# Kernel tuning notes

Hardware: AMD Instinct MI355X
Metric: run time of the kernel (lower is better)

## Reference

```python
import jax, jax.numpy as jnp
import numpy as np

NUM_HEADS = 4


def setup_inputs() -> dict:
    key = jax.random.key(0)
    ks = jax.random.split(key, 5)
    B, N, D = 4096, 49, 128  # B = batch(64) * num_windows(64), N = 7*7 window
    nW = 64
    x = jax.random.normal(ks[0], (B, N, D), dtype=jnp.float32)
    mask = jax.random.normal(ks[1], (nW, N, N), dtype=jnp.float32)
    w_qkv = jax.random.normal(ks[2], (3 * D, D), dtype=jnp.float32) * 0.02
    w_proj = jax.random.normal(ks[3], (D, D), dtype=jnp.float32) * 0.02
    b_proj = jax.random.normal(ks[4], (D,), dtype=jnp.float32) * 0.02
    return {"x": x, "mask": mask, "w_qkv": w_qkv, "w_proj": w_proj, "b_proj": b_proj}


def reference(x, mask, w_qkv, w_proj, b_proj):
    B, N, D = x.shape
    H = NUM_HEADS
    hd = D // H
    scale = hd ** (-0.5)
    # qkv projection (torch Linear: y = x @ W^T), no bias
    qkv = (x @ w_qkv.T).reshape(B, N, 3, H, hd)
    qkv = jnp.transpose(qkv, (2, 0, 3, 1, 4))  # [3, B, H, N, hd]
    q, k, v = qkv[0], qkv[1], qkv[2]
    attn = jnp.einsum("bhqd,bhkd->bhqk", q, k) * scale  # [B, H, N, N]
    nW = mask.shape[0]
    # add per-window additive mask, broadcast over batch and heads
    attn = attn.reshape(B // nW, nW, H, N, N) + mask[None, :, None, :, :]
    attn = attn.reshape(B, H, N, N)
    attn = jax.nn.softmax(attn, axis=-1)
    out = jnp.einsum("bhqk,bhkd->bhqd", attn, v)  # [B, H, N, hd]
    out = jnp.transpose(out, (0, 2, 1, 3)).reshape(B, N, D)
    return out @ w_proj.T + b_proj
```

## Files before the change

### kernel.cpp

```cpp
#include <hip/hip_runtime.h>
#include <hip/hip_bf16.h>

typedef _Float16 f16;
typedef __attribute__((ext_vector_type(8))) _Float16 f16x8;
typedef __attribute__((ext_vector_type(4))) _Float16 f16x4;
typedef __attribute__((ext_vector_type(4))) float f32x4;

#define MFMA16(a, b, c) __builtin_amdgcn_mfma_f32_16x16x32_f16((a), (b), (c), 0, 0, 0)

#define NWIN 4096
#define WPB 16

__global__ void cvt_weights(const float* __restrict__ wq,
                            const float* __restrict__ wp,
                            f16* __restrict__ o) {
    int i = blockIdx.x * blockDim.x + threadIdx.x;
    if (i < 49152) o[i] = (f16)wq[i];
    if (i < 16384) o[49152 + i] = (f16)wp[i];
}

__device__ inline f16x8 cvt8(const float* p) {
    float4 u0 = *(const float4*)p;
    float4 u1 = *(const float4*)(p + 4);
    f16x8 t;
    t[0] = (f16)u0.x; t[1] = (f16)u0.y; t[2] = (f16)u0.z; t[3] = (f16)u0.w;
    t[4] = (f16)u1.x; t[5] = (f16)u1.y; t[6] = (f16)u1.z; t[7] = (f16)u1.w;
    return t;
}

__global__ __launch_bounds__(512, 1)
void fused_all(const float* __restrict__ x, const float* __restrict__ mask,
               const f16* __restrict__ wq_h, const f16* __restrict__ wp_h,
               const float* __restrict__ bias, float* __restrict__ out) {
    __shared__ f16 xb[2][64 * 128];
    __shared__ f16 qlds[64 * 128];
    __shared__ f16 klds[64 * 128];
    __shared__ f16 vlds[128 * 64];
    __shared__ f16 scr[8][2048];

    const int tid = threadIdx.x;
    const int wave = tid >> 6;
    const int lane = tid & 63;
    const int lg = lane >> 4;
    const int lr = lane & 15;
    const int w0 = blockIdx.x * WPB;

    const int amt = wave & 3;
    const int ahh = wave >> 2;
    const int ar0 = amt * 16;

    f16* ps0 = scr[wave];
    f16* ps1 = scr[wave] + 1024;

    f16x8 bw[3][4];
#pragma unroll
    for (int j = 0; j < 3; ++j)
#pragma unroll
        for (int kc = 0; kc < 4; ++kc)
            bw[j][kc] = *(const f16x8*)&wq_h[((wave + 8 * j) * 16 + lr) * 128 + kc * 32 + 8 * lg];
    f16x8 wpr[4];
#pragma unroll
    for (int kc = 0; kc < 4; ++kc)
        wpr[kc] = *(const f16x8*)&wp_h[(wave * 16 + lr) * 128 + kc * 32 + 8 * lg];
    const float bc = bias[wave * 16 + lr];

    auto stage = [&](int w, int p) {
        const float* xw = x + (size_t)w * (49 * 128);
        for (int i = tid; i < 2048; i += 512) {
            const int row = i >> 5;
            const int c4 = (i & 31) << 2;
            float4 v = {0.f, 0.f, 0.f, 0.f};
            if (row < 49) v = ((const float4*)xw)[i];
            f16x4 t;
            t[0] = (f16)v.x; t[1] = (f16)v.y; t[2] = (f16)v.z; t[3] = (f16)v.w;
            *(f16x4*)&xb[p][row * 128 + (c4 ^ ((row & 7) << 3))] = t;
        }
    };

    stage(w0, 0);
    __syncthreads();

    const float sc = 0.17677669529663687f;

    for (int wi = 0; wi < WPB; ++wi) {
        const int w = w0 + wi;
        const int cur = wi & 1;
        if (wi < WPB - 1) stage(w + 1, cur ^ 1);

        const float* mw = mask + (size_t)(w & 63) * (49 * 49);
        float mv[4][4];
#pragma unroll
        for (int reg = 0; reg < 4; ++reg) {
            const int n = ar0 + 4 * lg + reg;
#pragma unroll
            for (int nt = 0; nt < 4; ++nt) {
                const int col = nt * 16 + lr;
                mv[reg][nt] = (n < 49 && col < 49) ? mw[n * 49 + col] : 0.f;
            }
        }

#pragma unroll
        for (int mt = 0; mt < 4; ++mt) {
            const int nb = mt * 16;
            f16x8 a[4];
#pragma unroll
            for (int kc = 0; kc < 4; ++kc)
                a[kc] = *(const f16x8*)&xb[cur][(nb + lr) * 128 + ((kc * 32 + 8 * lg) ^ ((lr & 7) << 3))];

#pragma unroll
            for (int j = 0; j < 3; ++j) {
                __builtin_amdgcn_s_setprio(1);
                f32x4 acc = {0.f, 0.f, 0.f, 0.f};
#pragma unroll
                for (int kc = 0; kc < 4; ++kc) acc = MFMA16(a[kc], bw[j][kc], acc);
                __builtin_amdgcn_s_setprio(0);

                const int c = wave * 16 + lr;
                if (j < 2) {
                    f16* dst = (j == 0) ? qlds : klds;
#pragma unroll
                    for (int reg = 0; reg < 4; ++reg) {
                        const int n = nb + 4 * lg + reg;
                        dst[n * 128 + (c ^ ((n & 7) << 3))] = (f16)acc[reg];
                    }
                } else {
#pragma unroll
                    for (int reg = 0; reg < 4; ++reg) {
                        const int n = nb + 4 * lg + reg;
                        vlds[c * 64 + (n ^ ((c & 7) << 3))] = (f16)acc[reg];
                    }
                }
            }
        }
        __syncthreads();

        const int h0 = 2 * ahh;
        const int h1 = 2 * ahh + 1;
        const int arow = ar0 + lr;

        f16x8 aq0 = *(const f16x8*)&qlds[arow * 128 + ((h0 * 32 + 8 * lg) ^ ((arow & 7) << 3))];
        f16x8 aq1 = *(const f16x8*)&qlds[arow * 128 + ((h1 * 32 + 8 * lg) ^ ((arow & 7) << 3))];

        f32x4 s0[4], s1[4];
        {
            __builtin_amdgcn_s_setprio(1);
#pragma unroll
            for (int nt = 0; nt < 4; ++nt) {
                const int krow = nt * 16 + lr;
                f16x8 bk = *(const f16x8*)&klds[krow * 128 + ((h0 * 32 + 8 * lg) ^ ((krow & 7) << 3))];
                f32x4 z = {0.f, 0.f, 0.f, 0.f};
                s0[nt] = MFMA16(aq0, bk, z);
            }
#pragma unroll
            for (int nt = 0; nt < 4; ++nt) {
                const int krow = nt * 16 + lr;
                f16x8 bk = *(const f16x8*)&klds[krow * 128 + ((h1 * 32 + 8 * lg) ^ ((krow & 7) << 3))];
                f32x4 z = {0.f, 0.f, 0.f, 0.f};
                s1[nt] = MFMA16(aq1, bk, z);
            }
            __builtin_amdgcn_s_setprio(0);
        }

        float lsum0[4], lsum1[4];
#pragma unroll
        for (int reg = 0; reg < 4; ++reg) {
            const int row = 4 * lg + reg;
            float sum0 = 0.f, sum1 = 0.f;
#pragma unroll
            for (int nt = 0; nt < 4; ++nt) {
                const int col = nt * 16 + lr;
                const int off = row * 64 + (col ^ ((row & 7) << 3));
                float e0 = (col < 49) ? __expf(s0[nt][reg] * sc + mv[reg][nt]) : 0.f;
                float e1 = (col < 49) ? __expf(s1[nt][reg] * sc + mv[reg][nt]) : 0.f;
                sum0 += e0;
                sum1 += e1;
                ps0[off] = (f16)e0;
                ps1[off] = (f16)e1;
            }
            lsum0[reg] = sum0;
            lsum1[reg] = sum1;
        }

        f16x8 bv0[2][2], bv1[2][2];
#pragma unroll
        for (int nt = 0; nt < 2; ++nt)
#pragma unroll
            for (int kc = 0; kc < 2; ++kc) {
                const int vr0 = h0 * 32 + nt * 16 + lr;
                const int vr1 = h1 * 32 + nt * 16 + lr;
                bv0[nt][kc] = *(const f16x8*)&vlds[vr0 * 64 + ((kc * 32 + 8 * lg) ^ ((vr0 & 7) << 3))];
                bv1[nt][kc] = *(const f16x8*)&vlds[vr1 * 64 + ((kc * 32 + 8 * lg) ^ ((vr1 & 7) << 3))];
            }

        f16x8 ap0[2], ap1[2];
#pragma unroll
        for (int kc = 0; kc < 2; ++kc) {
            const int off = lr * 64 + ((kc * 32 + 8 * lg) ^ ((lr & 7) << 3));
            ap0[kc] = *(const f16x8*)&ps0[off];
            ap1[kc] = *(const f16x8*)&ps1[off];
        }
        f32x4 o00 = {0.f, 0.f, 0.f, 0.f}, o01 = {0.f, 0.f, 0.f, 0.f};
        f32x4 o10 = {0.f, 0.f, 0.f, 0.f}, o11 = {0.f, 0.f, 0.f, 0.f};
        __builtin_amdgcn_s_setprio(1);
#pragma unroll
        for (int kc = 0; kc < 2; ++kc) {
            o00 = MFMA16(ap0[kc], bv0[0][kc], o00);
            o01 = MFMA16(ap0[kc], bv0[1][kc], o01);
            o10 = MFMA16(ap1[kc], bv1[0][kc], o10);
            o11 = MFMA16(ap1[kc], bv1[1][kc], o11);
        }
        __builtin_amdgcn_s_setprio(0);

#pragma unroll
        for (int reg = 0; reg < 4; ++reg) {
            float sum0 = lsum0[reg], sum1 = lsum1[reg];
            for (int d = 1; d < 16; d <<= 1) {
                sum0 += __shfl_xor(sum0, d, 64);
                sum1 += __shfl_xor(sum1, d, 64);
            }
            const float inv0 = __fdividef(1.f, sum0);
            const float inv1 = __fdividef(1.f, sum1);
            o00[reg] *= inv0;
            o01[reg] *= inv0;
            o10[reg] *= inv1;
            o11[reg] *= inv1;
        }

#pragma unroll
        for (int reg = 0; reg < 4; ++reg) {
            const int n = ar0 + 4 * lg + reg;
            const int s = (n & 7) << 3;
            qlds[n * 128 + ((h0 * 32 + lr) ^ s)] = (f16)o00[reg];
            qlds[n * 128 + ((h0 * 32 + 16 + lr) ^ s)] = (f16)o01[reg];
            qlds[n * 128 + ((h1 * 32 + lr) ^ s)] = (f16)o10[reg];
            qlds[n * 128 + ((h1 * 32 + 16 + lr) ^ s)] = (f16)o11[reg];
        }
        __syncthreads();

        float* ob = out + (size_t)w * (49 * 128);
#pragma unroll
        for (int mt = 0; mt < 4; ++mt) {
            const int prow = mt * 16 + lr;
            f16x8 aa[4];
#pragma unroll
            for (int kc = 0; kc < 4; ++kc)
                aa[kc] = *(const f16x8*)&qlds[prow * 128 + ((kc * 32 + 8 * lg) ^ ((prow & 7) << 3))];
            __builtin_amdgcn_s_setprio(1);
            f32x4 acc = {0.f, 0.f, 0.f, 0.f};
#pragma unroll
            for (int kc = 0; kc < 4; ++kc) acc = MFMA16(aa[kc], wpr[kc], acc);
            __builtin_amdgcn_s_setprio(0);

#pragma unroll
            for (int reg = 0; reg < 4; ++reg) {
                const int n = mt * 16 + 4 * lg + reg;
                if (n < 49) ob[n * 128 + wave * 16 + lr] = acc[reg] + bc;
            }
        }
        __syncthreads();
    }
}

template <bool WB>
__global__ __launch_bounds__(256, 4)
void fused_wattn(const float* __restrict__ x, const float* __restrict__ mask,
                 const float* __restrict__ wq_f, const float* __restrict__ wp_f,
                 const f16* __restrict__ wq_h, const f16* __restrict__ wp_h,
                 const float* __restrict__ bias, float* __restrict__ out) {
    __shared__ f16 ks[64 * 128];
    __shared__ f16 vt[128 * 64];
    __shared__ f16 scr[4][1024];

    const int b = blockIdx.x;
    const int wid = b & 63;
    const int tid = threadIdx.x;
    const int wave = tid >> 6;
    const int lane = tid & 63;
    const int lg = lane >> 4;
    const int lr = lane & 15;
    const int r0 = wave * 16;
    f16* ps = scr[wave];

    f16x8 a[4];
    {
        const int xrow = r0 + lr;
        if (xrow < 49) {
            const float* xp = x + ((size_t)b * 49 + xrow) * 128 + 8 * lg;
#pragma unroll
            for (int kc = 0; kc < 4; ++kc) a[kc] = cvt8(xp + kc * 32);
        } else {
            f16x8 z = {0, 0, 0, 0, 0, 0, 0, 0};
#pragma unroll
            for (int kc = 0; kc < 4; ++kc) a[kc] = z;
        }
    }

    float mv[4][4];
#pragma unroll
    for (int reg = 0; reg < 4; ++reg) {
        const int n = r0 + 4 * lg + reg;
#pragma unroll
        for (int nt = 0; nt < 4; ++nt) {
            const int col = nt * 16 + lr;
            mv[reg][nt] = (n < 49 && col < 49) ? mask[((size_t)wid * 49 + n) * 49 + col] : 0.f;
        }
    }

    f16x4 qd[8];
#pragma unroll
    for (int ct = 0; ct < 24; ++ct) {
        const int wrow = ct * 16 + lr;
        f16x8 bw[4];
        if (WB) {
#pragma unroll
            for (int kc = 0; kc < 4; ++kc)
                bw[kc] = *(const f16x8*)&wq_h[wrow * 128 + kc * 32 + 8 * lg];
        } else {
#pragma unroll
            for (int kc = 0; kc < 4; ++kc)
                bw[kc] = cvt8(&wq_f[wrow * 128 + kc * 32 + 8 * lg]);
        }
        f32x4 acc = {0.f, 0.f, 0.f, 0.f};
#pragma unroll
        for (int kc = 0; kc < 4; ++kc) acc = MFMA16(a[kc], bw[kc], acc);

        if (ct < 8) {
            f16x4 q;
#pragma unroll
            for (int reg = 0; reg < 4; ++reg) q[reg] = (f16)acc[reg];
            qd[ct] = q;
        } else if (ct < 16) {
#pragma unroll
            for (int reg = 0; reg < 4; ++reg) {
                const int n = r0 + 4 * lg + reg;
                const int c = wrow - 128;
                ks[n * 128 + (c ^ ((n & 7) << 3))] = (f16)acc[reg];
            }
        } else {
#pragma unroll
            for (int reg = 0; reg < 4; ++reg) {
                const int n = r0 + 4 * lg + reg;
                const int dch = wrow - 256;
                vt[dch * 64 + (n ^ ((dch & 7) << 3))] = (f16)acc[reg];
            }
        }
    }
    __syncthreads();

    const float sc = 0.17677669529663687f;
    f32x4 oacc[4][2];

#pragma unroll
    for (int h = 0; h < 4; ++h) {
#pragma unroll
        for (int c2 = 0; c2 < 2; ++c2)
#pragma unroll
            for (int reg = 0; reg < 4; ++reg) {
                const int row = 4 * lg + reg;
                const int col = c2 * 16 + lr;
                ps[row * 32 + (col ^ ((row & 3) << 3))] = qd[2 * h + c2][reg];
            }
        f16x8 aq = *(const f16x8*)&ps[lr * 32 + ((8 * lg) ^ ((lr & 3) << 3))];

        f32x4 s[4];
#pragma unroll
        for (int nt = 0; nt < 4; ++nt) {
            const int krow = nt * 16 + lr;
            f16x8 bk = *(const f16x8*)&ks[krow * 128 + ((h * 32 + 8 * lg) ^ ((krow & 7) << 3))];
            f32x4 z = {0.f, 0.f, 0.f, 0.f};
            s[nt] = MFMA16(aq, bk, z);
        }

#pragma unroll
        for (int reg = 0; reg < 4; ++reg) {
            float vals[4];
            float sum = 0.f;
#pragma unroll
            for (int nt = 0; nt < 4; ++nt) {
                const int col = nt * 16 + lr;
                float e = (col < 49) ? __expf(s[nt][reg] * sc + mv[reg][nt]) : 0.f;
                vals[nt] = e;
                sum += e;
            }
            for (int d = 1; d < 16; d <<= 1) sum += __shfl_xor(sum, d, 64);
            const float inv = __fdividef(1.f, sum);
            const int row = 4 * lg + reg;
#pragma unroll
            for (int nt = 0; nt < 4; ++nt) {
                const int col = nt * 16 + lr;
                ps[row * 64 + (col ^ ((row & 7) << 3))] = (f16)(vals[nt] * inv);
            }
        }

        f16x8 ap[2];
#pragma unroll
        for (int kc = 0; kc < 2; ++kc)
            ap[kc] = *(const f16x8*)&ps[lr * 64 + ((kc * 32 + 8 * lg) ^ ((lr & 7) << 3))];
#pragma unroll
        for (int nt = 0; nt < 2; ++nt) {
            const int vrow = h * 32 + nt * 16 + lr;
            f32x4 acc = {0.f, 0.f, 0.f, 0.f};
#pragma unroll
            for (int kc = 0; kc < 2; ++kc) {
                f16x8 bv = *(const f16x8*)&vt[vrow * 64 + ((kc * 32 + 8 * lg) ^ ((vrow & 7) << 3))];
                acc = MFMA16(ap[kc], bv, acc);
            }
            oacc[h][nt] = acc;
        }
    }

    f16x8 aa[4];
#pragma unroll
    for (int pass = 0; pass < 2; ++pass) {
#pragma unroll
        for (int h2 = 0; h2 < 2; ++h2)
#pragma unroll
            for (int nt = 0; nt < 2; ++nt)
#pragma unroll
                for (int reg = 0; reg < 4; ++reg) {
                    const int row = 4 * lg + reg;
                    const int col = h2 * 32 + nt * 16 + lr;
                    ps[row * 64 + (col ^ ((row & 7) << 3))] = (f16)oacc[pass * 2 + h2][nt][reg];
                }
#pragma unroll
        for (int kcg = 0; kcg < 2; ++kcg)
            aa[pass * 2 + kcg] = *(const f16x8*)&ps[lr * 64 + ((kcg * 32 + 8 * lg) ^ ((lr & 7) << 3))];
    }

    float* ob = out + (size_t)b * (49 * 128);
#pragma unroll
    for (int ct = 0; ct < 8; ++ct) {
        const int wrow = ct * 16 + lr;
        f16x8 bw[4];
        if (WB) {
#pragma unroll
            for (int kc = 0; kc < 4; ++kc)
                bw[kc] = *(const f16x8*)&wq_h[wrow * 128 + kc * 32 + 8 * lg];
        } else {
#pragma unroll
            for (int kc = 0; kc < 4; ++kc)
                bw[kc] = cvt8(&wp_f[wrow * 128 + kc * 32 + 8 * lg]);
        }
        f32x4 acc = {0.f, 0.f, 0.f, 0.f};
#pragma unroll
        for (int kc = 0; kc < 4; ++kc) acc = MFMA16(aa[kc], bw[kc], acc);

        const float bc = bias[wrow];
#pragma unroll
        for (int reg = 0; reg < 4; ++reg) {
            const int n = r0 + 4 * lg + reg;
            if (n < 49) ob[n * 128 + ct * 16 + lr] = acc[reg] + bc;
        }
    }
}

extern "C" void kernel_launch(void* const* d_in, const int* in_sizes, int n_in,
                              void* d_out, int out_size, void* d_ws, size_t ws_size,
                              hipStream_t stream) {
    const float* x = (const float*)d_in[0];
    const float* mask = (const float*)d_in[1];
    const float* wq = (const float*)d_in[2];
    const float* wp = (const float*)d_in[3];
    const float* bp = (const float*)d_in[4];
    float* out = (float*)d_out;

    const size_t need_wb = (size_t)(49152 + 16384) * sizeof(f16);

    if (ws_size >= need_wb && d_ws != nullptr) {
        f16* wsh = (f16*)d_ws;
        cvt_weights<<<192, 256, 0, stream>>>(wq, wp, wsh);
        fused_all<<<NWIN / WPB, 512, 0, stream>>>(x, mask, wsh, wsh + 49152, bp, out);
    } else {
        fused_wattn<false><<<4096, 256, 0, stream>>>(x, mask, wq, wp, nullptr, nullptr, bp, out);
    }
}
```

Baseline: 108.4 us.

## Process two windows per iteration with double-buffered Q/K/V LDS

```diff
diff --git a/kernel.cpp b/kernel.cpp
--- a/kernel.cpp
+++ b/kernel.cpp
@@ -32,10 +32,10 @@
 void fused_all(const float* __restrict__ x, const float* __restrict__ mask,
                const f16* __restrict__ wq_h, const f16* __restrict__ wp_h,
                const float* __restrict__ bias, float* __restrict__ out) {
-    __shared__ f16 xb[2][64 * 128];
-    __shared__ f16 qlds[64 * 128];
-    __shared__ f16 klds[64 * 128];
-    __shared__ f16 vlds[128 * 64];
+    __shared__ f16 xb[2][50 * 128];
+    __shared__ f16 qlds[2][64 * 128];
+    __shared__ f16 klds[2][64 * 128];
+    __shared__ f16 vlds[2][128 * 64];
     __shared__ f16 scr[8][2048];
 
     const int tid = threadIdx.x;
@@ -66,11 +66,10 @@
 
     auto stage = [&](int w, int p) {
         const float* xw = x + (size_t)w * (49 * 128);
-        for (int i = tid; i < 2048; i += 512) {
+        for (int i = tid; i < 1568; i += 512) {
             const int row = i >> 5;
             const int c4 = (i & 31) << 2;
-            float4 v = {0.f, 0.f, 0.f, 0.f};
-            if (row < 49) v = ((const float4*)xw)[i];
+            float4 v = ((const float4*)xw)[i];
             f16x4 t;
             t[0] = (f16)v.x; t[1] = (f16)v.y; t[2] = (f16)v.z; t[3] = (f16)v.w;
             *(f16x4*)&xb[p][row * 128 + (c4 ^ ((row & 7) << 3))] = t;
@@ -78,183 +77,209 @@
     };
 
     stage(w0, 0);
+    stage(w0 + 1, 1);
     __syncthreads();
 
     const float sc = 0.17677669529663687f;
 
-    for (int wi = 0; wi < WPB; ++wi) {
-        const int w = w0 + wi;
-        const int cur = wi & 1;
-        if (wi < WPB - 1) stage(w + 1, cur ^ 1);
-
-        const float* mw = mask + (size_t)(w & 63) * (49 * 49);
-        float mv[4][4];
-#pragma unroll
-        for (int reg = 0; reg < 4; ++reg) {
-            const int n = ar0 + 4 * lg + reg;
+    for (int pi = 0; pi < WPB / 2; ++pi) {
+        const int wp0 = w0 + 2 * pi;
+
+        float mv[2][4][4];
+#pragma unroll
+        for (int ws = 0; ws < 2; ++ws) {
+            const float* mw = mask + (size_t)((wp0 + ws) & 63) * (49 * 49);
+#pragma unroll
+            for (int reg = 0; reg < 4; ++reg) {
+                const int n = ar0 + 4 * lg + reg;
+#pragma unroll
+                for (int nt = 0; nt < 4; ++nt) {
+                    const int col = nt * 16 + lr;
+                    mv[ws][reg][nt] = (n < 49 && col < 49) ? mw[n * 49 + col] : 0.f;
+                }
+            }
+        }
+
+#pragma unroll
+        for (int ws = 0; ws < 2; ++ws) {
+#pragma unroll
+            for (int mt = 0; mt < 4; ++mt) {
+                const int nb = mt * 16;
+                const int xrow = nb + lr;
+                f16x8 a[4];
+                if (xrow < 49) {
+#pragma unroll
+                    for (int kc = 0; kc < 4; ++kc)
+                        a[kc] = *(const f16x8*)&xb[ws][xrow * 128 + ((kc * 32 + 8 * lg) ^ ((xrow & 7) << 3))];
+                } else {
+                    f16x8 z = {0, 0, 0, 0, 0, 0, 0, 0};
+#pragma unroll
+                    for (int kc = 0; kc < 4; ++kc) a[kc] = z;
+                }
+
+#pragma unroll
+                for (int j = 0; j < 3; ++j) {
+                    __builtin_amdgcn_s_setprio(1);
+                    f32x4 acc = {0.f, 0.f, 0.f, 0.f};
+#pragma unroll
+                    for (int kc = 0; kc < 4; ++kc) acc = MFMA16(a[kc], bw[j][kc], acc);
+                    __builtin_amdgcn_s_setprio(0);
+
+                    const int c = wave * 16 + lr;
+                    if (j < 2) {
+                        f16* dst = (j == 0) ? qlds[ws] : klds[ws];
+#pragma unroll
+                        for (int reg = 0; reg < 4; ++reg) {
+                            const int n = nb + 4 * lg + reg;
+                            dst[n * 128 + (c ^ ((n & 7) << 3))] = (f16)acc[reg];
+                        }
+                    } else {
+#pragma unroll
+                        for (int reg = 0; reg < 4; ++reg) {
+                            const int n = nb + 4 * lg + reg;
+                            vlds[ws][c * 64 + (n ^ ((c & 7) << 3))] = (f16)acc[reg];
+                        }
+                    }
+                }
+            }
+        }
+        __syncthreads();
+
+        if (pi + 1 < WPB / 2) {
+            stage(wp0 + 2, 0);
+            stage(wp0 + 3, 1);
+        }
+
+#pragma unroll
+        for (int ws = 0; ws < 2; ++ws) {
+            const int h0 = 2 * ahh;
+            const int h1 = 2 * ahh + 1;
+            const int arow = ar0 + lr;
+            const f16* ql = qlds[ws];
+            const f16* kl = klds[ws];
+            const f16* vl = vlds[ws];
+
+            f16x8 aq0 = *(const f16x8*)&ql[arow * 128 + ((h0 * 32 + 8 * lg) ^ ((arow & 7) << 3))];
+            f16x8 aq1 = *(const f16x8*)&ql[arow * 128 + ((h1 * 32 + 8 * lg) ^ ((arow & 7) << 3))];
+
+            f32x4 s0[4], s1[4];
+            __builtin_amdgcn_s_setprio(1);
 #pragma unroll
             for (int nt = 0; nt < 4; ++nt) {
-                const int col = nt * 16 + lr;
-                mv[reg][nt] = (n < 49 && col < 49) ? mw[n * 49 + col] : 0.f;
-            }
-        }
-
-#pragma unroll
-        for (int mt = 0; mt < 4; ++mt) {
-            const int nb = mt * 16;
-            f16x8 a[4];
-#pragma unroll
-            for (int kc = 0; kc < 4; ++kc)
-                a[kc] = *(const f16x8*)&xb[cur][(nb + lr) * 128 + ((kc * 32 + 8 * lg) ^ ((lr & 7) << 3))];
-
-#pragma unroll
-            for (int j = 0; j < 3; ++j) {
+                const int krow = nt * 16 + lr;
+                f16x8 bk = *(const f16x8*)&kl[krow * 128 + ((h0 * 32 + 8 * lg) ^ ((krow & 7) << 3))];
+                f32x4 z = {0.f, 0.f, 0.f, 0.f};
+                s0[nt] = MFMA16(aq0, bk, z);
+            }
+#pragma unroll
+            for (int nt = 0; nt < 4; ++nt) {
+                const int krow = nt * 16 + lr;
+                f16x8 bk = *(const f16x8*)&kl[krow * 128 + ((h1 * 32 + 8 * lg) ^ ((krow & 7) << 3))];
+                f32x4 z = {0.f, 0.f, 0.f, 0.f};
+                s1[nt] = MFMA16(aq1, bk, z);
+            }
+            __builtin_amdgcn_s_setprio(0);
+
+            float lsum0[4], lsum1[4];
+#pragma unroll
+            for (int reg = 0; reg < 4; ++reg) {
+                const int row = 4 * lg + reg;
+                float sum0 = 0.f, sum1 = 0.f;
+#pragma unroll
+                for (int nt = 0; nt < 4; ++nt) {
+                    const int col = nt * 16 + lr;
+                    const int off = row * 64 + (col ^ ((row & 7) << 3));
+                    float e0 = (col < 49) ? __expf(s0[nt][reg] * sc + mv[ws][reg][nt]) : 0.f;
+                    float e1 = (col < 49) ? __expf(s1[nt][reg] * sc + mv[ws][reg][nt]) : 0.f;
+                    sum0 += e0;
+                    sum1 += e1;
+                    ps0[off] = (f16)e0;
+                    ps1[off] = (f16)e1;
+                }
+                lsum0[reg] = sum0;
+                lsum1[reg] = sum1;
+            }
+
+            f16x8 bv0[2][2], bv1[2][2];
+#pragma unroll
+            for (int nt = 0; nt < 2; ++nt)
+#pragma unroll
+                for (int kc = 0; kc < 2; ++kc) {
+                    const int vr0 = h0 * 32 + nt * 16 + lr;
+                    const int vr1 = h1 * 32 + nt * 16 + lr;
+                    bv0[nt][kc] = *(const f16x8*)&vl[vr0 * 64 + ((kc * 32 + 8 * lg) ^ ((vr0 & 7) << 3))];
+                    bv1[nt][kc] = *(const f16x8*)&vl[vr1 * 64 + ((kc * 32 + 8 * lg) ^ ((vr1 & 7) << 3))];
+                }
+
+            f16x8 ap0[2], ap1[2];
+#pragma unroll
+            for (int kc = 0; kc < 2; ++kc) {
+                const int off = lr * 64 + ((kc * 32 + 8 * lg) ^ ((lr & 7) << 3));
+                ap0[kc] = *(const f16x8*)&ps0[off];
+                ap1[kc] = *(const f16x8*)&ps1[off];
+            }
+            f32x4 o00 = {0.f, 0.f, 0.f, 0.f}, o01 = {0.f, 0.f, 0.f, 0.f};
+            f32x4 o10 = {0.f, 0.f, 0.f, 0.f}, o11 = {0.f, 0.f, 0.f, 0.f};
+            __builtin_amdgcn_s_setprio(1);
+#pragma unroll
+            for (int kc = 0; kc < 2; ++kc) {
+                o00 = MFMA16(ap0[kc], bv0[0][kc], o00);
+                o01 = MFMA16(ap0[kc], bv0[1][kc], o01);
+                o10 = MFMA16(ap1[kc], bv1[0][kc], o10);
+                o11 = MFMA16(ap1[kc], bv1[1][kc], o11);
+            }
+            __builtin_amdgcn_s_setprio(0);
+
+#pragma unroll
+            for (int reg = 0; reg < 4; ++reg) {
+                float sum0 = lsum0[reg], sum1 = lsum1[reg];
+                for (int d = 1; d < 16; d <<= 1) {
+                    sum0 += __shfl_xor(sum0, d, 64);
+                    sum1 += __shfl_xor(sum1, d, 64);
+                }
+                const float inv0 = __fdividef(1.f, sum0);
+                const float inv1 = __fdividef(1.f, sum1);
+                o00[reg] *= inv0;
+                o01[reg] *= inv0;
+                o10[reg] *= inv1;
+                o11[reg] *= inv1;
+            }
+
+            f16* qw = qlds[ws];
+#pragma unroll
+            for (int reg = 0; reg < 4; ++reg) {
+                const int n = ar0 + 4 * lg + reg;
+                const int s = (n & 7) << 3;
+                qw[n * 128 + ((h0 * 32 + lr) ^ s)] = (f16)o00[reg];
+                qw[n * 128 + ((h0 * 32 + 16 + lr) ^ s)] = (f16)o01[reg];
+                qw[n * 128 + ((h1 * 32 + lr) ^ s)] = (f16)o10[reg];
+                qw[n * 128 + ((h1 * 32 + 16 + lr) ^ s)] = (f16)o11[reg];
+            }
+        }
+        __syncthreads();
+
+#pragma unroll
+        for (int ws = 0; ws < 2; ++ws) {
+            const f16* qw = qlds[ws];
+            float* ob = out + (size_t)(wp0 + ws) * (49 * 128);
+#pragma unroll
+            for (int mt = 0; mt < 4; ++mt) {
+                const int prow = mt * 16 + lr;
+                f16x8 aa[4];
+#pragma unroll
+                for (int kc = 0; kc < 4; ++kc)
+                    aa[kc] = *(const f16x8*)&qw[prow * 128 + ((kc * 32 + 8 * lg) ^ ((prow & 7) << 3))];
                 __builtin_amdgcn_s_setprio(1);
                 f32x4 acc = {0.f, 0.f, 0.f, 0.f};
 #pragma unroll
-                for (int kc = 0; kc < 4; ++kc) acc = MFMA16(a[kc], bw[j][kc], acc);
+                for (int kc = 0; kc < 4; ++kc) acc = MFMA16(aa[kc], wpr[kc], acc);
                 __builtin_amdgcn_s_setprio(0);
 
-                const int c = wave * 16 + lr;
-                if (j < 2) {
-                    f16* dst = (j == 0) ? qlds : klds;
-#pragma unroll
-                    for (int reg = 0; reg < 4; ++reg) {
-                        const int n = nb + 4 * lg + reg;
-                        dst[n * 128 + (c ^ ((n & 7) << 3))] = (f16)acc[reg];
-                    }
-                } else {
-#pragma unroll
-                    for (int reg = 0; reg < 4; ++reg) {
-                        const int n = nb + 4 * lg + reg;
-                        vlds[c * 64 + (n ^ ((c & 7) << 3))] = (f16)acc[reg];
-                    }
-                }
-            }
-        }
-        __syncthreads();
-
-        const int h0 = 2 * ahh;
-        const int h1 = 2 * ahh + 1;
-        const int arow = ar0 + lr;
-
-        f16x8 aq0 = *(const f16x8*)&qlds[arow * 128 + ((h0 * 32 + 8 * lg) ^ ((arow & 7) << 3))];
-        f16x8 aq1 = *(const f16x8*)&qlds[arow * 128 + ((h1 * 32 + 8 * lg) ^ ((arow & 7) << 3))];
-
-        f32x4 s0[4], s1[4];
-        {
-            __builtin_amdgcn_s_setprio(1);
-#pragma unroll
-            for (int nt = 0; nt < 4; ++nt) {
-                const int krow = nt * 16 + lr;
-                f16x8 bk = *(const f16x8*)&klds[krow * 128 + ((h0 * 32 + 8 * lg) ^ ((krow & 7) << 3))];
-                f32x4 z = {0.f, 0.f, 0.f, 0.f};
-                s0[nt] = MFMA16(aq0, bk, z);
-            }
-#pragma unroll
-            for (int nt = 0; nt < 4; ++nt) {
-                const int krow = nt * 16 + lr;
-                f16x8 bk = *(const f16x8*)&klds[krow * 128 + ((h1 * 32 + 8 * lg) ^ ((krow & 7) << 3))];
-                f32x4 z = {0.f, 0.f, 0.f, 0.f};
-                s1[nt] = MFMA16(aq1, bk, z);
-            }
-            __builtin_amdgcn_s_setprio(0);
-        }
-
-        float lsum0[4], lsum1[4];
-#pragma unroll
-        for (int reg = 0; reg < 4; ++reg) {
-            const int row = 4 * lg + reg;
-            float sum0 = 0.f, sum1 = 0.f;
-#pragma unroll
-            for (int nt = 0; nt < 4; ++nt) {
-                const int col = nt * 16 + lr;
-                const int off = row * 64 + (col ^ ((row & 7) << 3));
-                float e0 = (col < 49) ? __expf(s0[nt][reg] * sc + mv[reg][nt]) : 0.f;
-                float e1 = (col < 49) ? __expf(s1[nt][reg] * sc + mv[reg][nt]) : 0.f;
-                sum0 += e0;
-                sum1 += e1;
-                ps0[off] = (f16)e0;
-                ps1[off] = (f16)e1;
-            }
-            lsum0[reg] = sum0;
-            lsum1[reg] = sum1;
-        }
-
-        f16x8 bv0[2][2], bv1[2][2];
-#pragma unroll
-        for (int nt = 0; nt < 2; ++nt)
-#pragma unroll
-            for (int kc = 0; kc < 2; ++kc) {
-                const int vr0 = h0 * 32 + nt * 16 + lr;
-                const int vr1 = h1 * 32 + nt * 16 + lr;
-                bv0[nt][kc] = *(const f16x8*)&vlds[vr0 * 64 + ((kc * 32 + 8 * lg) ^ ((vr0 & 7) << 3))];
-                bv1[nt][kc] = *(const f16x8*)&vlds[vr1 * 64 + ((kc * 32 + 8 * lg) ^ ((vr1 & 7) << 3))];
-            }
-
-        f16x8 ap0[2], ap1[2];
-#pragma unroll
-        for (int kc = 0; kc < 2; ++kc) {
-            const int off = lr * 64 + ((kc * 32 + 8 * lg) ^ ((lr & 7) << 3));
-            ap0[kc] = *(const f16x8*)&ps0[off];
-            ap1[kc] = *(const f16x8*)&ps1[off];
-        }
-        f32x4 o00 = {0.f, 0.f, 0.f, 0.f}, o01 = {0.f, 0.f, 0.f, 0.f};
-        f32x4 o10 = {0.f, 0.f, 0.f, 0.f}, o11 = {0.f, 0.f, 0.f, 0.f};
-        __builtin_amdgcn_s_setprio(1);
-#pragma unroll
-        for (int kc = 0; kc < 2; ++kc) {
-            o00 = MFMA16(ap0[kc], bv0[0][kc], o00);
-            o01 = MFMA16(ap0[kc], bv0[1][kc], o01);
-            o10 = MFMA16(ap1[kc], bv1[0][kc], o10);
-            o11 = MFMA16(ap1[kc], bv1[1][kc], o11);
-        }
-        __builtin_amdgcn_s_setprio(0);
-
-#pragma unroll
-        for (int reg = 0; reg < 4; ++reg) {
-            float sum0 = lsum0[reg], sum1 = lsum1[reg];
-            for (int d = 1; d < 16; d <<= 1) {
-                sum0 += __shfl_xor(sum0, d, 64);
-                sum1 += __shfl_xor(sum1, d, 64);
-            }
-            const float inv0 = __fdividef(1.f, sum0);
-            const float inv1 = __fdividef(1.f, sum1);
-            o00[reg] *= inv0;
-            o01[reg] *= inv0;
-            o10[reg] *= inv1;
-            o11[reg] *= inv1;
-        }
-
-#pragma unroll
-        for (int reg = 0; reg < 4; ++reg) {
-            const int n = ar0 + 4 * lg + reg;
-            const int s = (n & 7) << 3;
-            qlds[n * 128 + ((h0 * 32 + lr) ^ s)] = (f16)o00[reg];
-            qlds[n * 128 + ((h0 * 32 + 16 + lr) ^ s)] = (f16)o01[reg];
-            qlds[n * 128 + ((h1 * 32 + lr) ^ s)] = (f16)o10[reg];
-            qlds[n * 128 + ((h1 * 32 + 16 + lr) ^ s)] = (f16)o11[reg];
-        }
-        __syncthreads();
-
-        float* ob = out + (size_t)w * (49 * 128);
-#pragma unroll
-        for (int mt = 0; mt < 4; ++mt) {
-            const int prow = mt * 16 + lr;
-            f16x8 aa[4];
-#pragma unroll
-            for (int kc = 0; kc < 4; ++kc)
-                aa[kc] = *(const f16x8*)&qlds[prow * 128 + ((kc * 32 + 8 * lg) ^ ((prow & 7) << 3))];
-            __builtin_amdgcn_s_setprio(1);
-            f32x4 acc = {0.f, 0.f, 0.f, 0.f};
-#pragma unroll
-            for (int kc = 0; kc < 4; ++kc) acc = MFMA16(aa[kc], wpr[kc], acc);
-            __builtin_amdgcn_s_setprio(0);
-
-#pragma unroll
-            for (int reg = 0; reg < 4; ++reg) {
-                const int n = mt * 16 + 4 * lg + reg;
-                if (n < 49) ob[n * 128 + wave * 16 + lr] = acc[reg] + bc;
+#pragma unroll
+                for (int reg = 0; reg < 4; ++reg) {
+                    const int n = mt * 16 + 4 * lg + reg;
+                    if (n < 49) ob[n * 128 + wave * 16 + lr] = acc[reg] + bc;
+                }
             }
         }
         __syncthreads();
@@ -435,7 +460,7 @@
         if (WB) {
 #pragma unroll
             for (int kc = 0; kc < 4; ++kc)
-                bw[kc] = *(const f16x8*)&wq_h[wrow * 128 + kc * 32 + 8 * lg];
+                bw[kc] = *(const f16x8*)&wp_h[wrow * 128 + kc * 32 + 8 * lg];
         } else {
 #pragma unroll
             for (int kc = 0; kc < 4; ++kc)
```

Result: slower. 187.3 us (+72.8%).

## Double-buffer Q/K/V LDS tiles and drop trailing per-window barrier

Applied to the files above, without the earlier changes.

```diff
diff --git a/kernel.cpp b/kernel.cpp
--- a/kernel.cpp
+++ b/kernel.cpp
@@ -32,10 +32,10 @@
 void fused_all(const float* __restrict__ x, const float* __restrict__ mask,
                const f16* __restrict__ wq_h, const f16* __restrict__ wp_h,
                const float* __restrict__ bias, float* __restrict__ out) {
-    __shared__ f16 xb[2][64 * 128];
-    __shared__ f16 qlds[64 * 128];
-    __shared__ f16 klds[64 * 128];
-    __shared__ f16 vlds[128 * 64];
+    __shared__ f16 xb[2][50 * 128];
+    __shared__ f16 qlds[2][64 * 128];
+    __shared__ f16 klds[2][64 * 128];
+    __shared__ f16 vlds[2][128 * 64];
     __shared__ f16 scr[8][2048];
 
     const int tid = threadIdx.x;
@@ -66,11 +66,10 @@
 
     auto stage = [&](int w, int p) {
         const float* xw = x + (size_t)w * (49 * 128);
-        for (int i = tid; i < 2048; i += 512) {
+        for (int i = tid; i < 1568; i += 512) {
             const int row = i >> 5;
             const int c4 = (i & 31) << 2;
-            float4 v = {0.f, 0.f, 0.f, 0.f};
-            if (row < 49) v = ((const float4*)xw)[i];
+            float4 v = ((const float4*)xw)[i];
             f16x4 t;
             t[0] = (f16)v.x; t[1] = (f16)v.y; t[2] = (f16)v.z; t[3] = (f16)v.w;
             *(f16x4*)&xb[p][row * 128 + (c4 ^ ((row & 7) << 3))] = t;
@@ -99,13 +98,23 @@
             }
         }
 
+        f16* ql = qlds[cur];
+        f16* kl = klds[cur];
+        f16* vl = vlds[cur];
 #pragma unroll
         for (int mt = 0; mt < 4; ++mt) {
             const int nb = mt * 16;
+            const int xrow = nb + lr;
             f16x8 a[4];
-#pragma unroll
-            for (int kc = 0; kc < 4; ++kc)
-                a[kc] = *(const f16x8*)&xb[cur][(nb + lr) * 128 + ((kc * 32 + 8 * lg) ^ ((lr & 7) << 3))];
+            if (xrow < 49) {
+#pragma unroll
+                for (int kc = 0; kc < 4; ++kc)
+                    a[kc] = *(const f16x8*)&xb[cur][xrow * 128 + ((kc * 32 + 8 * lg) ^ ((xrow & 7) << 3))];
+            } else {
+                f16x8 z = {0, 0, 0, 0, 0, 0, 0, 0};
+#pragma unroll
+                for (int kc = 0; kc < 4; ++kc) a[kc] = z;
+            }
 
 #pragma unroll
             for (int j = 0; j < 3; ++j) {
@@ -117,7 +126,7 @@
 
                 const int c = wave * 16 + lr;
                 if (j < 2) {
-                    f16* dst = (j == 0) ? qlds : klds;
+                    f16* dst = (j == 0) ? ql : kl;
 #pragma unroll
                     for (int reg = 0; reg < 4; ++reg) {
                         const int n = nb + 4 * lg + reg;
@@ -127,7 +136,7 @@
 #pragma unroll
                     for (int reg = 0; reg < 4; ++reg) {
                         const int n = nb + 4 * lg + reg;
-                        vlds[c * 64 + (n ^ ((c & 7) << 3))] = (f16)acc[reg];
+                        vl[c * 64 + (n ^ ((c & 7) << 3))] = (f16)acc[reg];
                     }
                 }
             }
@@ -138,8 +147,8 @@
         const int h1 = 2 * ahh + 1;
         const int arow = ar0 + lr;
 
-        f16x8 aq0 = *(const f16x8*)&qlds[arow * 128 + ((h0 * 32 + 8 * lg) ^ ((arow & 7) << 3))];
-        f16x8 aq1 = *(const f16x8*)&qlds[arow * 128 + ((h1 * 32 + 8 * lg) ^ ((arow & 7) << 3))];
+        f16x8 aq0 = *(const f16x8*)&ql[arow * 128 + ((h0 * 32 + 8 * lg) ^ ((arow & 7) << 3))];
+        f16x8 aq1 = *(const f16x8*)&ql[arow * 128 + ((h1 * 32 + 8 * lg) ^ ((arow & 7) << 3))];
 
         f32x4 s0[4], s1[4];
         {
@@ -147,14 +156,14 @@
 #pragma unroll
             for (int nt = 0; nt < 4; ++nt) {
                 const int krow = nt * 16 + lr;
-                f16x8 bk = *(const f16x8*)&klds[krow * 128 + ((h0 * 32 + 8 * lg) ^ ((krow & 7) << 3))];
+                f16x8 bk = *(const f16x8*)&kl[krow * 128 + ((h0 * 32 + 8 * lg) ^ ((krow & 7) << 3))];
                 f32x4 z = {0.f, 0.f, 0.f, 0.f};
                 s0[nt] = MFMA16(aq0, bk, z);
             }
 #pragma unroll
             for (int nt = 0; nt < 4; ++nt) {
                 const int krow = nt * 16 + lr;
-                f16x8 bk = *(const f16x8*)&klds[krow * 128 + ((h1 * 32 + 8 * lg) ^ ((krow & 7) << 3))];
+                f16x8 bk = *(const f16x8*)&kl[krow * 128 + ((h1 * 32 + 8 * lg) ^ ((krow & 7) << 3))];
                 f32x4 z = {0.f, 0.f, 0.f, 0.f};
                 s1[nt] = MFMA16(aq1, bk, z);
             }
@@ -188,8 +197,8 @@
             for (int kc = 0; kc < 2; ++kc) {
                 const int vr0 = h0 * 32 + nt * 16 + lr;
                 const int vr1 = h1 * 32 + nt * 16 + lr;
-                bv0[nt][kc] = *(const f16x8*)&vlds[vr0 * 64 + ((kc * 32 + 8 * lg) ^ ((vr0 & 7) << 3))];
-                bv1[nt][kc] = *(const f16x8*)&vlds[vr1 * 64 + ((kc * 32 + 8 * lg) ^ ((vr1 & 7) << 3))];
+                bv0[nt][kc] = *(const f16x8*)&vl[vr0 * 64 + ((kc * 32 + 8 * lg) ^ ((vr0 & 7) << 3))];
+                bv1[nt][kc] = *(const f16x8*)&vl[vr1 * 64 + ((kc * 32 + 8 * lg) ^ ((vr1 & 7) << 3))];
             }
 
         f16x8 ap0[2], ap1[2];
@@ -230,10 +239,10 @@
         for (int reg = 0; reg < 4; ++reg) {
             const int n = ar0 + 4 * lg + reg;
             const int s = (n & 7) << 3;
-            qlds[n * 128 + ((h0 * 32 + lr) ^ s)] = (f16)o00[reg];
-            qlds[n * 128 + ((h0 * 32 + 16 + lr) ^ s)] = (f16)o01[reg];
-            qlds[n * 128 + ((h1 * 32 + lr) ^ s)] = (f16)o10[reg];
-            qlds[n * 128 + ((h1 * 32 + 16 + lr) ^ s)] = (f16)o11[reg];
+            ql[n * 128 + ((h0 * 32 + lr) ^ s)] = (f16)o00[reg];
+            ql[n * 128 + ((h0 * 32 + 16 + lr) ^ s)] = (f16)o01[reg];
+            ql[n * 128 + ((h1 * 32 + lr) ^ s)] = (f16)o10[reg];
+            ql[n * 128 + ((h1 * 32 + 16 + lr) ^ s)] = (f16)o11[reg];
         }
         __syncthreads();
 
@@ -244,7 +253,7 @@
             f16x8 aa[4];
 #pragma unroll
             for (int kc = 0; kc < 4; ++kc)
-                aa[kc] = *(const f16x8*)&qlds[prow * 128 + ((kc * 32 + 8 * lg) ^ ((prow & 7) << 3))];
+                aa[kc] = *(const f16x8*)&ql[prow * 128 + ((kc * 32 + 8 * lg) ^ ((prow & 7) << 3))];
             __builtin_amdgcn_s_setprio(1);
             f32x4 acc = {0.f, 0.f, 0.f, 0.f};
 #pragma unroll
@@ -257,7 +266,6 @@
                 if (n < 49) ob[n * 128 + wave * 16 + lr] = acc[reg] + bc;
             }
         }
-        __syncthreads();
     }
 }
 
```

Measured after the change: 107.2 us. Within noise of the previous version (-1.1%).
